# Performance work log

Hardware: AMD Instinct MI355X
Metric: run time of the kernel (lower is better)

Reference implementation:

```python
import jax, jax.numpy as jnp
import numpy as np

D = 512

def setup_inputs() -> dict:
    key = jax.random.key(0)
    k1, k2, k3, k4 = jax.random.split(key, 4)
    inputs = jax.random.normal(k1, (8, 2048, D), dtype=jnp.float32)
    # torch nn.Linear weights are [out, in]; y = x @ W.T
    Wk = jax.random.normal(k2, (D, D), dtype=jnp.float32) / np.sqrt(D)
    Wq = jax.random.normal(k3, (D, D), dtype=jnp.float32) / np.sqrt(D)
    Wv = jax.random.normal(k4, (D, D), dtype=jnp.float32) / np.sqrt(D)
    return {"inputs": inputs, "Wk": Wk, "Wq": Wq, "Wv": Wv}

def reference(inputs, Wk, Wq, Wv):
    # q/k/v: [B, S, D]
    q = jnp.einsum('bsd,ed->bse', inputs, Wq)
    k = jnp.einsum('bsd,ed->bse', inputs, Wk)
    v = jnp.einsum('bsd,ed->bse', inputs, Wv)
    scores = jnp.einsum('bqd,bkd->bqk', q, k) * 5.0  # note: scale is *5, not 1/sqrt(d)
    attn = jax.nn.softmax(scores, axis=-1)
    # dropout is identity in eval mode
    out = jnp.einsum('bqk,bkd->bqd', attn, v)
    return jnp.swapaxes(out, -2, -1)  # [B, D, S]
```

## Files before the change

kernel.cpp:

```cpp
#include <hip/hip_runtime.h>
#include <stdint.h>

typedef __attribute__((ext_vector_type(4))) float f32x4;
typedef __attribute__((ext_vector_type(8))) short short8;
typedef unsigned short u16;
typedef unsigned int u32;

#define DEV static __device__ __forceinline__

DEV u32 fbits(float f) { union { float f; u32 u; } v; v.f = f; return v.u; }
DEV float bits2f(u32 u) { union { u32 u; float f; } v; v.u = u; return v.f; }

DEV u16 f2bf_rne(float f) {
  u32 u = fbits(f);
  u32 r = u + 0x7fffu + ((u >> 16) & 1u);
  return (u16)(r >> 16);
}
DEV u16 f2bf_trunc(float f) { return (u16)(fbits(f) >> 16); }
DEV float bf2f(u16 h) { return bits2f(((u32)h) << 16); }

DEV void split2(float f, u16& h, u16& l) {
  h = f2bf_rne(f);
  float r = f - bf2f(h);
  l = f2bf_trunc(r);
}

DEV void gll16(const void* gsrc, char* ldsp) {
  __builtin_amdgcn_global_load_lds(
      (const __attribute__((address_space(1))) u32*)gsrc,
      (__attribute__((address_space(3))) u32*)ldsp,
      16, 0, 0);
}

DEV f32x4 mfma16(short8 a, short8 b, f32x4 c) {
  return __builtin_amdgcn_mfma_f32_16x16x32_bf16(a, b, c, 0, 0, 0);
}

template<int EPI>
__global__ __launch_bounds__(256, 1) void proj_gemm(
    const float* __restrict__ A, const float* __restrict__ Bm,
    u16* __restrict__ o0, u16* __restrict__ o1, float scale)
{
  extern __shared__ char smem[];
  const int tid = threadIdx.x;
  const int lane = tid & 63, wv = tid >> 6;
  const int wm = wv & 1, wn = wv >> 1;
  const int lm = lane & 15, lg = lane >> 4;
  const int n0 = blockIdx.x * 128, m0 = blockIdx.y * 128;

  f32x4 acc[4][4] = {};

  for (int k0 = 0; k0 < 512; k0 += 64) {
    __syncthreads();
    #pragma unroll
    for (int i = 0; i < 8; ++i) {
      int c = i * 256 + tid;
      int row = c >> 4, c4 = c & 15;
      f32x4 av = *(const f32x4*)(A + (size_t)(m0 + row) * 512 + (k0 + c4 * 4));
      f32x4 bv = *(const f32x4*)(Bm + (size_t)(n0 + row) * 512 + (k0 + c4 * 4));
      int base = row * 128 + ((((c4 >> 1) ^ (row & 7)) << 4) + (c4 & 1) * 8);
      u16 ah[4], al[4], bh[4], bl[4];
      #pragma unroll
      for (int j = 0; j < 4; ++j) { split2(av[j], ah[j], al[j]); split2(bv[j], bh[j], bl[j]); }
      *(ushort4*)(smem +         base) = make_ushort4(ah[0], ah[1], ah[2], ah[3]);
      *(ushort4*)(smem + 16384 + base) = make_ushort4(al[0], al[1], al[2], al[3]);
      *(ushort4*)(smem + 32768 + base) = make_ushort4(bh[0], bh[1], bh[2], bh[3]);
      *(ushort4*)(smem + 49152 + base) = make_ushort4(bl[0], bl[1], bl[2], bl[3]);
    }
    __syncthreads();
    #pragma unroll
    for (int ks = 0; ks < 2; ++ks) {
      short8 fah[4], fal[4], fbh[4], fbl[4];
      #pragma unroll
      for (int t = 0; t < 4; ++t) {
        int ar = wm * 64 + t * 16 + lm;
        int ac = (((ks * 4 + lg) ^ (ar & 7)) << 4);
        fah[t] = *(const short8*)(smem +         ar * 128 + ac);
        fal[t] = *(const short8*)(smem + 16384 + ar * 128 + ac);
        int br = wn * 64 + t * 16 + lm;
        int bc = (((ks * 4 + lg) ^ (br & 7)) << 4);
        fbh[t] = *(const short8*)(smem + 32768 + br * 128 + bc);
        fbl[t] = *(const short8*)(smem + 49152 + br * 128 + bc);
      }
      #pragma unroll
      for (int mt = 0; mt < 4; ++mt)
        #pragma unroll
        for (int nt = 0; nt < 4; ++nt) {
          acc[mt][nt] = mfma16(fah[mt], fbh[nt], acc[mt][nt]);
          acc[mt][nt] = mfma16(fah[mt], fbl[nt], acc[mt][nt]);
          acc[mt][nt] = mfma16(fal[mt], fbh[nt], acc[mt][nt]);
        }
    }
  }
  #pragma unroll
  for (int mt = 0; mt < 4; ++mt)
    #pragma unroll
    for (int nt = 0; nt < 4; ++nt)
      #pragma unroll
      for (int i = 0; i < 4; ++i) {
        float v = acc[mt][nt][i] * scale;
        int m = m0 + wm * 64 + mt * 16 + lg * 4 + i;
        int n = n0 + wn * 64 + nt * 16 + lm;
        if (EPI == 0) {
          u16 h, l; split2(v, h, l);
          o0[(size_t)m * 512 + n] = h;
          o1[(size_t)m * 512 + n] = l;
        } else {
          int r = n & 31;
          int cc = ((r >> 2) & 3) * 8 + ((r >> 4) << 2) + (r & 3);
          int n2 = (n & ~31) | cc;
          size_t addr = ((size_t)(n >> 11) << 20) | ((size_t)m << 11) | (size_t)(n2 & 2047);
          o0[addr] = f2bf_rne(v);
        }
      }
}

#define STG_BASE 65536

DEV void stage_chunk(const u16* __restrict__ kh, const u16* __restrict__ kl,
                     const u16* __restrict__ vt, char* smem, int g, int buf,
                     int b, int kt, int c, int tid256) {
  char* dst = smem + STG_BASE + g * 49152 + buf * 16384;
  if (c < 8) {
    const size_t kbase = (size_t)b * 2048 * 512 + (size_t)kt * 64 * 512 + c * 64;
    #pragma unroll
    for (int j = 0; j < 2; ++j) {
      int slot = j * 256 + tid256;
      int r = slot >> 3, ch = slot & 7, sc = ch ^ (r & 7);
      size_t src = kbase + (size_t)r * 512 + sc * 8;
      gll16(kh + src, dst + slot * 16);
      gll16(kl + src, dst + 8192 + slot * 16);
    }
  } else {
    const int cv = c - 8;
    const size_t vbase = (size_t)b * 512 * 2048 + (size_t)(cv * 128) * 2048 + (size_t)kt * 64;
    #pragma unroll
    for (int j = 0; j < 4; ++j) {
      int slot = j * 256 + tid256;
      int r = slot >> 3, ch = slot & 7, sc = ch ^ (r & 7);
      gll16(vt + vbase + (size_t)r * 2048 + sc * 8, dst + slot * 16);
    }
  }
}

__global__ __launch_bounds__(512, 2) void attn_fused(
    const u16* __restrict__ qh, const u16* __restrict__ ql,
    const u16* __restrict__ kh, const u16* __restrict__ kl,
    const u16* __restrict__ vt, float* __restrict__ out)
{
  extern __shared__ char smem[];
  const int tid = threadIdx.x;
  const int lane = tid & 63, wv = tid >> 6;
  const int g = wv >> 2, wg = wv & 3;
  const int lm = lane & 15, lg = lane >> 4;
  const int tid256 = tid & 255;
  const int b = blockIdx.x, qt = blockIdx.y;
  const int qrow = wg * 16 + lm;

  const size_t qbase = (size_t)(b * 2048 + qt * 64) * 512;
  #pragma unroll
  for (int it = 0; it < 8; ++it) {
    int slot = it * 512 + tid;
    int row = slot >> 6, ch = slot & 63;
    int sc = ch ^ (row & 7);
    gll16(qh + qbase + (size_t)row * 512 + sc * 8, smem + slot * 16);
  }
  short8 qlr[16];
  #pragma unroll
  for (int j = 0; j < 16; ++j)
    qlr[j] = *(const short8*)(ql + qbase + (size_t)qrow * 512 + j * 32 + lg * 8);

  stage_chunk(kh, kl, vt, smem, g, 0, b, g, 0, tid256);
  stage_chunk(kh, kl, vt, smem, g, 1, b, g, 1, tid256);

  float m = -3e38f, l = 0.f;
  f32x4 oacc[32] = {};
  short8 pb0 = {}, pb1 = {};

  for (int t = 0; t < 16; ++t) {
    f32x4 sacc[4] = {};
    #pragma unroll
    for (int c = 0; c < 12; ++c) {
      {
        int nc = c + 2, tt = t;
        if (nc >= 12) { nc -= 12; tt = t + 1; }
        int nkt = 2 * (tt & 15) + g;
        stage_chunk(kh, kl, vt, smem, g, (c + 2) % 3, b, nkt, nc, tid256);
      }
      if (c == 8) {
        float mx = fmaxf(fmaxf(fmaxf(sacc[0][0], sacc[0][1]), fmaxf(sacc[0][2], sacc[0][3])),
                         fmaxf(fmaxf(sacc[1][0], sacc[1][1]), fmaxf(sacc[1][2], sacc[1][3])));
        mx = fmaxf(mx, fmaxf(fmaxf(fmaxf(sacc[2][0], sacc[2][1]), fmaxf(sacc[2][2], sacc[2][3])),
                             fmaxf(fmaxf(sacc[3][0], sacc[3][1]), fmaxf(sacc[3][2], sacc[3][3]))));
        mx = fmaxf(mx, __shfl_xor(mx, 16, 64));
        mx = fmaxf(mx, __shfl_xor(mx, 32, 64));
        if (__any(mx > m)) {
          float mn = fmaxf(m, mx);
          float alpha = __expf(m - mn);
          m = mn;
          #pragma unroll
          for (int f = 0; f < 32; ++f) {
            oacc[f][0] *= alpha; oacc[f][1] *= alpha;
            oacc[f][2] *= alpha; oacc[f][3] *= alpha;
          }
          l *= alpha;
        }
        float sm = 0.f;
        #pragma unroll
        for (int t4 = 0; t4 < 4; ++t4)
          #pragma unroll
          for (int i = 0; i < 4; ++i) {
            float p = __expf(sacc[t4][i] - m);
            sacc[t4][i] = p;
            sm += p;
          }
        sm += __shfl_xor(sm, 16, 64);
        sm += __shfl_xor(sm, 32, 64);
        l += sm;
        #pragma unroll
        for (int j = 0; j < 4; ++j) {
          pb0[j]     = (short)f2bf_rne(sacc[0][j]);
          pb0[4 + j] = (short)f2bf_rne(sacc[1][j]);
          pb1[j]     = (short)f2bf_rne(sacc[2][j]);
          pb1[4 + j] = (short)f2bf_rne(sacc[3][j]);
        }
      }
      asm volatile("s_waitcnt vmcnt(8)" ::: "memory");
      __builtin_amdgcn_s_barrier();
      __builtin_amdgcn_sched_barrier(0);
      const char* bufp = smem + STG_BASE + g * 49152 + (c % 3) * 16384;
      __builtin_amdgcn_s_setprio(1);
      if (c < 8) {
        #pragma unroll
        for (int ks = 0; ks < 2; ++ks) {
          int qg = c * 8 + ks * 4 + lg;
          short8 bqh = *(const short8*)(smem + qrow * 1024 + ((qg ^ (qrow & 7)) << 4));
          short8 bql = qlr[c * 2 + ks];
          #pragma unroll
          for (int t4 = 0; t4 < 4; ++t4) {
            int krow = t4 * 16 + lm;
            int kc = ((ks * 4 + lg) ^ (krow & 7)) << 4;
            short8 akh = *(const short8*)(bufp + krow * 128 + kc);
            short8 akl = *(const short8*)(bufp + 8192 + krow * 128 + kc);
            sacc[t4] = mfma16(akh, bqh, sacc[t4]);
            sacc[t4] = mfma16(akh, bql, sacc[t4]);
            sacc[t4] = mfma16(akl, bqh, sacc[t4]);
          }
        }
      } else {
        const int cv = c - 8;
        #pragma unroll
        for (int dt = 0; dt < 8; ++dt) {
          int vrow = dt * 16 + lm;
          short8 av0 = *(const short8*)(bufp + vrow * 128 + ((lg ^ (vrow & 7)) << 4));
          short8 av1 = *(const short8*)(bufp + vrow * 128 + (((4 + lg) ^ (vrow & 7)) << 4));
          f32x4 o = oacc[cv * 8 + dt];
          o = mfma16(av0, pb0, o);
          o = mfma16(av1, pb1, o);
          oacc[cv * 8 + dt] = o;
        }
      }
      __builtin_amdgcn_s_setprio(0);
      __builtin_amdgcn_sched_barrier(0);
      __builtin_amdgcn_s_barrier();
    }
  }
  asm volatile("s_waitcnt vmcnt(0)" ::: "memory");
  __syncthreads();
  float* mlp = (float*)(smem + 131072);
  if (g == 1) {
    const int base = wg * 32768;
    #pragma unroll
    for (int f = 0; f < 32; ++f) {
      int d4 = (f * 16 + lg * 4) * 4;
      *(f32x4*)(smem + base + lm * 2048 + (d4 ^ ((lm & 7) << 4))) = oacc[f];
    }
    if (lg == 0) {
      mlp[(wg * 16 + lm) * 2 + 0] = m;
      mlp[(wg * 16 + lm) * 2 + 1] = l;
    }
  }
  __syncthreads();
  if (g == 0) {
    float m1 = mlp[(wg * 16 + lm) * 2 + 0];
    float l1 = mlp[(wg * 16 + lm) * 2 + 1];
    float mf = fmaxf(m, m1);
    float a0 = __expf(m - mf), a1 = __expf(m1 - mf);
    float linv = 1.0f / (a0 * l + a1 * l1);
    const int s = qt * 64 + wg * 16 + lm;
    float* ob = out + ((size_t)b << 20) + s;
    #pragma unroll
    for (int f = 0; f < 32; ++f) {
      int d4 = (f * 16 + lg * 4) * 4;
      f32x4 o1 = *(const f32x4*)(smem + wg * 32768 + lm * 2048 + (d4 ^ ((lm & 7) << 4)));
      #pragma unroll
      for (int i = 0; i < 4; ++i) {
        int d = f * 16 + lg * 4 + i;
        ob[(size_t)d * 2048] = (a0 * oacc[f][i] + a1 * o1[i]) * linv;
      }
    }
  }
}

extern "C" void kernel_launch(void* const* d_in, const int* in_sizes, int n_in,
                              void* d_out, int out_size, void* d_ws, size_t ws_size,
                              hipStream_t stream) {
  (void)in_sizes; (void)n_in; (void)out_size; (void)ws_size;
  const float* x  = (const float*)d_in[0];
  const float* Wk = (const float*)d_in[1];
  const float* Wq = (const float*)d_in[2];
  const float* Wv = (const float*)d_in[3];
  float* out = (float*)d_out;

  const size_t SZ = (size_t)16384 * 512;
  u16* q_hi = (u16*)d_ws;
  u16* q_lo = q_hi + SZ;
  u16* k_hi = q_lo + SZ;
  u16* k_lo = k_hi + SZ;
  u16* v_t  = k_lo + SZ;

  (void)hipFuncSetAttribute(reinterpret_cast<const void*>(&proj_gemm<0>),
                            hipFuncAttributeMaxDynamicSharedMemorySize, 65536);
  (void)hipFuncSetAttribute(reinterpret_cast<const void*>(&proj_gemm<1>),
                            hipFuncAttributeMaxDynamicSharedMemorySize, 65536);
  (void)hipFuncSetAttribute(reinterpret_cast<const void*>(&attn_fused),
                            hipFuncAttributeMaxDynamicSharedMemorySize, 163840);

  dim3 pblk(256), ablk(512);
  proj_gemm<0><<<dim3(4, 128), pblk, 65536, stream>>>(x, Wq, q_hi, q_lo, 5.0f);
  proj_gemm<0><<<dim3(4, 128), pblk, 65536, stream>>>(x, Wk, k_hi, k_lo, 1.0f);
  proj_gemm<1><<<dim3(128, 4), pblk, 65536, stream>>>(Wv, x, v_t, nullptr, 1.0f);
  attn_fused<<<dim3(8, 32), ablk, 163840, stream>>>(q_hi, q_lo, k_hi, k_lo, v_t, out);
}
```

Before: 366.8 us.

## Use per-group LDS counter barriers with smaller staging chunks in fused attention

```diff
diff --git a/kernel.cpp b/kernel.cpp
--- a/kernel.cpp
+++ b/kernel.cpp
@@ -116,26 +116,36 @@
 }
 
 #define STG_BASE 65536
-
-DEV void stage_chunk(const u16* __restrict__ kh, const u16* __restrict__ kl,
-                     const u16* __restrict__ vt, char* smem, int g, int buf,
-                     int b, int kt, int c, int tid256) {
-  char* dst = smem + STG_BASE + g * 49152 + buf * 16384;
-  if (c < 8) {
-    const size_t kbase = (size_t)b * 2048 * 512 + (size_t)kt * 64 * 512 + c * 64;
+#define CNT_OFF  131072
+#define MLP_OFF  131584
+#define LDS_SZ   132096
+
+DEV void group_bar(char* smem, int g, int lane, int target) {
+  int* ca = (int*)(smem + CNT_OFF + g * 4);
+  if (lane == 0) atomicAdd(ca, 1);
+  volatile int* cp = (volatile int*)ca;
+  int v = *cp;
+  while (v < target) { __builtin_amdgcn_s_sleep(1); v = *cp; }
+}
+
+DEV void stage_chunk8(const u16* __restrict__ kh, const u16* __restrict__ kl,
+                      const u16* __restrict__ vt, char* smem, int g, int buf,
+                      int b, int kt, int c, int tid256) {
+  char* dst = smem + STG_BASE + g * 24576 + buf * 8192;
+  if (c < 16) {
+    const u16* src = (c & 1) ? kl : kh;
+    const size_t kbase = (size_t)b * 2048 * 512 + (size_t)kt * 64 * 512 + (c >> 1) * 64;
     #pragma unroll
     for (int j = 0; j < 2; ++j) {
       int slot = j * 256 + tid256;
       int r = slot >> 3, ch = slot & 7, sc = ch ^ (r & 7);
-      size_t src = kbase + (size_t)r * 512 + sc * 8;
-      gll16(kh + src, dst + slot * 16);
-      gll16(kl + src, dst + 8192 + slot * 16);
+      gll16(src + kbase + (size_t)r * 512 + sc * 8, dst + slot * 16);
     }
   } else {
-    const int cv = c - 8;
-    const size_t vbase = (size_t)b * 512 * 2048 + (size_t)(cv * 128) * 2048 + (size_t)kt * 64;
-    #pragma unroll
-    for (int j = 0; j < 4; ++j) {
+    const int cv = c - 16;
+    const size_t vbase = (size_t)b * 512 * 2048 + (size_t)(cv * 64) * 2048 + (size_t)kt * 64;
+    #pragma unroll
+    for (int j = 0; j < 2; ++j) {
       int slot = j * 256 + tid256;
       int r = slot >> 3, ch = slot & 7, sc = ch ^ (r & 7);
       gll16(vt + vbase + (size_t)r * 2048 + sc * 8, dst + slot * 16);
@@ -157,6 +167,8 @@
   const int b = blockIdx.x, qt = blockIdx.y;
   const int qrow = wg * 16 + lm;
 
+  if (tid < 2) *((int*)(smem + CNT_OFF) + tid) = 0;
+
   const size_t qbase = (size_t)(b * 2048 + qt * 64) * 512;
   #pragma unroll
   for (int it = 0; it < 8; ++it) {
@@ -170,24 +182,26 @@
   for (int j = 0; j < 16; ++j)
     qlr[j] = *(const short8*)(ql + qbase + (size_t)qrow * 512 + j * 32 + lg * 8);
 
-  stage_chunk(kh, kl, vt, smem, g, 0, b, g, 0, tid256);
-  stage_chunk(kh, kl, vt, smem, g, 1, b, g, 1, tid256);
+  stage_chunk8(kh, kl, vt, smem, g, 0, b, g, 0, tid256);
+  asm volatile("s_waitcnt vmcnt(0)" ::: "memory");
+  __syncthreads();
 
   float m = -3e38f, l = 0.f;
   f32x4 oacc[32] = {};
   short8 pb0 = {}, pb1 = {};
+  int barn = 0;
 
   for (int t = 0; t < 16; ++t) {
     f32x4 sacc[4] = {};
     #pragma unroll
-    for (int c = 0; c < 12; ++c) {
+    for (int c = 0; c < 24; ++c) {
       {
-        int nc = c + 2, tt = t;
-        if (nc >= 12) { nc -= 12; tt = t + 1; }
+        int nc = c + 1, tt = t;
+        if (nc == 24) { nc = 0; ++tt; }
         int nkt = 2 * (tt & 15) + g;
-        stage_chunk(kh, kl, vt, smem, g, (c + 2) % 3, b, nkt, nc, tid256);
-      }
-      if (c == 8) {
+        stage_chunk8(kh, kl, vt, smem, g, (c + 1) % 3, b, nkt, nc, tid256);
+      }
+      if (c == 16) {
         float mx = fmaxf(fmaxf(fmaxf(sacc[0][0], sacc[0][1]), fmaxf(sacc[0][2], sacc[0][3])),
                          fmaxf(fmaxf(sacc[1][0], sacc[1][1]), fmaxf(sacc[1][2], sacc[1][3])));
         mx = fmaxf(mx, fmaxf(fmaxf(fmaxf(sacc[2][0], sacc[2][1]), fmaxf(sacc[2][2], sacc[2][3])),
@@ -225,49 +239,63 @@
           pb1[4 + j] = (short)f2bf_rne(sacc[3][j]);
         }
       }
-      asm volatile("s_waitcnt vmcnt(8)" ::: "memory");
-      __builtin_amdgcn_s_barrier();
+      asm volatile("s_waitcnt vmcnt(2)" ::: "memory");
+      ++barn;
+      group_bar(smem, g, lane, barn * 4);
       __builtin_amdgcn_sched_barrier(0);
-      const char* bufp = smem + STG_BASE + g * 49152 + (c % 3) * 16384;
+      const char* bufp = smem + STG_BASE + g * 24576 + (c % 3) * 8192;
       __builtin_amdgcn_s_setprio(1);
-      if (c < 8) {
+      if (c < 16) {
+        const int dc = c >> 1;
+        if (!(c & 1)) {
+          #pragma unroll
+          for (int ks = 0; ks < 2; ++ks) {
+            int qg = dc * 8 + ks * 4 + lg;
+            short8 bqh = *(const short8*)(smem + qrow * 1024 + ((qg ^ (qrow & 7)) << 4));
+            short8 bql = qlr[dc * 2 + ks];
+            #pragma unroll
+            for (int t4 = 0; t4 < 4; ++t4) {
+              int krow = t4 * 16 + lm;
+              int kc = ((ks * 4 + lg) ^ (krow & 7)) << 4;
+              short8 akh = *(const short8*)(bufp + krow * 128 + kc);
+              sacc[t4] = mfma16(akh, bqh, sacc[t4]);
+              sacc[t4] = mfma16(akh, bql, sacc[t4]);
+            }
+          }
+        } else {
+          #pragma unroll
+          for (int ks = 0; ks < 2; ++ks) {
+            int qg = dc * 8 + ks * 4 + lg;
+            short8 bqh = *(const short8*)(smem + qrow * 1024 + ((qg ^ (qrow & 7)) << 4));
+            #pragma unroll
+            for (int t4 = 0; t4 < 4; ++t4) {
+              int krow = t4 * 16 + lm;
+              int kc = ((ks * 4 + lg) ^ (krow & 7)) << 4;
+              short8 akl = *(const short8*)(bufp + krow * 128 + kc);
+              sacc[t4] = mfma16(akl, bqh, sacc[t4]);
+            }
+          }
+        }
+      } else {
+        const int cv = c - 16;
         #pragma unroll
-        for (int ks = 0; ks < 2; ++ks) {
-          int qg = c * 8 + ks * 4 + lg;
-          short8 bqh = *(const short8*)(smem + qrow * 1024 + ((qg ^ (qrow & 7)) << 4));
-          short8 bql = qlr[c * 2 + ks];
-          #pragma unroll
-          for (int t4 = 0; t4 < 4; ++t4) {
-            int krow = t4 * 16 + lm;
-            int kc = ((ks * 4 + lg) ^ (krow & 7)) << 4;
-            short8 akh = *(const short8*)(bufp + krow * 128 + kc);
-            short8 akl = *(const short8*)(bufp + 8192 + krow * 128 + kc);
-            sacc[t4] = mfma16(akh, bqh, sacc[t4]);
-            sacc[t4] = mfma16(akh, bql, sacc[t4]);
-            sacc[t4] = mfma16(akl, bqh, sacc[t4]);
-          }
-        }
-      } else {
-        const int cv = c - 8;
-        #pragma unroll
-        for (int dt = 0; dt < 8; ++dt) {
+        for (int dt = 0; dt < 4; ++dt) {
           int vrow = dt * 16 + lm;
           short8 av0 = *(const short8*)(bufp + vrow * 128 + ((lg ^ (vrow & 7)) << 4));
           short8 av1 = *(const short8*)(bufp + vrow * 128 + (((4 + lg) ^ (vrow & 7)) << 4));
-          f32x4 o = oacc[cv * 8 + dt];
+          f32x4 o = oacc[cv * 4 + dt];
           o = mfma16(av0, pb0, o);
           o = mfma16(av1, pb1, o);
-          oacc[cv * 8 + dt] = o;
+          oacc[cv * 4 + dt] = o;
         }
       }
       __builtin_amdgcn_s_setprio(0);
       __builtin_amdgcn_sched_barrier(0);
-      __builtin_amdgcn_s_barrier();
     }
   }
   asm volatile("s_waitcnt vmcnt(0)" ::: "memory");
   __syncthreads();
-  float* mlp = (float*)(smem + 131072);
+  float* mlp = (float*)(smem + MLP_OFF);
   if (g == 1) {
     const int base = wg * 32768;
     #pragma unroll
@@ -324,11 +352,11 @@
   (void)hipFuncSetAttribute(reinterpret_cast<const void*>(&proj_gemm<1>),
                             hipFuncAttributeMaxDynamicSharedMemorySize, 65536);
   (void)hipFuncSetAttribute(reinterpret_cast<const void*>(&attn_fused),
-                            hipFuncAttributeMaxDynamicSharedMemorySize, 163840);
+                            hipFuncAttributeMaxDynamicSharedMemorySize, LDS_SZ);
 
   dim3 pblk(256), ablk(512);
   proj_gemm<0><<<dim3(4, 128), pblk, 65536, stream>>>(x, Wq, q_hi, q_lo, 5.0f);
   proj_gemm<0><<<dim3(4, 128), pblk, 65536, stream>>>(x, Wk, k_hi, k_lo, 1.0f);
   proj_gemm<1><<<dim3(128, 4), pblk, 65536, stream>>>(Wv, x, v_t, nullptr, 1.0f);
-  attn_fused<<<dim3(8, 32), ablk, 163840, stream>>>(q_hi, q_lo, k_hi, k_lo, v_t, out);
-}
+  attn_fused<<<dim3(8, 32), ablk, LDS_SZ, stream>>>(q_hi, q_lo, k_hi, k_lo, v_t, out);
+}
```

After: 441.8 us. +20.4%, slower.
